# Kernel tuning notes

Hardware: AMD Instinct MI355X
Metric: run time of the kernel (lower is better)

The kernel has to match this reference:

```python
import jax, jax.numpy as jnp
import numpy as np

N_CLS = 8192
FEAT_DIM = 512
BATCH = 1024
PROTO_M = 0.95
TEMPERATURE = 0.1
BASE_TEMPERATURE = 0.1
EPS = 1e-12  # F.normalize eps


def setup_inputs() -> dict:
    key = jax.random.key(0)
    k1, k2, k3 = jax.random.split(key, 3)
    features = jax.random.normal(k1, (BATCH, FEAT_DIM), dtype=jnp.float32)
    features = features / jnp.maximum(jnp.linalg.norm(features, axis=1, keepdims=True), EPS)
    labels = jax.random.randint(k2, (BATCH,), 0, N_CLS, dtype=jnp.int64 if jax.config.jax_enable_x64 else jnp.int32)
    prototypes = jax.random.normal(k3, (N_CLS, FEAT_DIM), dtype=jnp.float32)
    prototypes = prototypes / jnp.maximum(jnp.linalg.norm(prototypes, axis=1, keepdims=True), EPS)
    return {"features": features, "labels": labels, "prototypes": prototypes}


def _l2norm_vec(v):
    # F.normalize(v, dim=0) for a 1-D vector
    return v / jnp.maximum(jnp.linalg.norm(v), EPS)


def reference(features, labels, prototypes):
    # --- sequential per-sample EMA prototype update (order matters) ---
    def step(protos, fl):
        f, l = fl
        new_p = _l2norm_vec(protos[l] * PROTO_M + f * (1.0 - PROTO_M))
        return protos.at[l].set(new_p), None

    protos, _ = jax.lax.scan(step, prototypes, (features, labels))

    # --- dispersion loss over prototype pairs ---
    logits = (protos @ protos.T) / TEMPERATURE            # [n_cls, n_cls]
    n = protos.shape[0]
    mask = 1.0 - jnp.eye(n, dtype=logits.dtype)           # off-diagonal pairs
    # log of mean exp over negatives (exactly the original, non-stabilized, form;
    # prototypes are unit-norm so |logits| <= 1/T and exp is safe)
    mean_prob_neg = jnp.log((mask * jnp.exp(logits)).sum(axis=1) / mask.sum(axis=1))
    # original drops NaN rows; with n_cls > 1 mask.sum(1) == n_cls-1 > 0 so none occur
    loss = (TEMPERATURE / BASE_TEMPERATURE) * mean_prob_neg.mean()
    return loss
```

## Files before the change

### kernel.cpp

```cpp
#include <hip/hip_runtime.h>
#include <hip/hip_fp8.h>
#include <stdint.h>

#define N_CLS 8192
#define FEAT  512
#define BATCH 1024
#define NTI   32
#define NTJ   64
#define NBLK  1056
#define NSLOT 8
#define SLOTB 24576

typedef __attribute__((ext_vector_type(4))) float f32x4;
typedef __attribute__((ext_vector_type(2))) long longx2;

__device__ inline unsigned char f2fp8(float x) {
    __hip_fp8_e4m3 q(x);
    return q.__x;
}

__global__ __launch_bounds__(256) void ema_kernel(
    const float* __restrict__ features, const int* __restrict__ labels,
    const float* __restrict__ protos,
    unsigned char* __restrict__ Phi8, float* __restrict__ rowsum) {
    const int row  = blockIdx.x * 4 + (threadIdx.x >> 6);
    const int lane = threadIdx.x & 63;
    if (lane == 0) rowsum[row] = 0.f;

    f32x4 p0 = *(const f32x4*)&protos[(size_t)row * FEAT + lane * 8];
    f32x4 p1 = *(const f32x4*)&protos[(size_t)row * FEAT + lane * 8 + 4];

    for (int c = 0; c < BATCH / 64; ++c) {
        int lab = labels[c * 64 + lane];
        unsigned long long m = __ballot(lab == row);
        while (m) {
            int b = __builtin_ctzll(m);
            m &= m - 1;
            int s = c * 64 + b;
            f32x4 f0 = *(const f32x4*)&features[(size_t)s * FEAT + lane * 8];
            f32x4 f1 = *(const f32x4*)&features[(size_t)s * FEAT + lane * 8 + 4];
            p0 = p0 * 0.95f + f0 * 0.05f;
            p1 = p1 * 0.95f + f1 * 0.05f;
            float ss = p0[0]*p0[0] + p0[1]*p0[1] + p0[2]*p0[2] + p0[3]*p0[3]
                     + p1[0]*p1[0] + p1[1]*p1[1] + p1[2]*p1[2] + p1[3]*p1[3];
            #pragma unroll
            for (int off = 32; off; off >>= 1) ss += __shfl_xor(ss, off);
            float inv = 1.0f / fmaxf(sqrtf(ss), 1e-12f);
            p0 *= inv; p1 *= inv;
        }
    }
    unsigned long long packed = 0;
    #pragma unroll
    for (int jj = 0; jj < 4; ++jj)
        packed |= (unsigned long long)f2fp8(p0[jj]) << (8 * jj);
    #pragma unroll
    for (int jj = 0; jj < 4; ++jj)
        packed |= (unsigned long long)f2fp8(p1[jj]) << (8 * (jj + 4));
    *(unsigned long long*)&Phi8[(size_t)row * FEAT + lane * 8] = packed;
}

__global__ __launch_bounds__(512, 4) void gemm_disp_kernel(
    const unsigned char* __restrict__ Phi8, float* __restrict__ rowsum) {
    __shared__ __align__(16) char smem[3 * SLOTB];

    int bid = blockIdx.x;
    int u = (bid & 7) * (NBLK / 8) + (bid >> 3);
    int i = 0;
    while (u >= NTJ - 2 * i) { u -= NTJ - 2 * i; ++i; }
    const int j = 2 * i + u;
    const bool diagovl = ((j >> 1) == i);

    const int w    = threadIdx.x >> 6;
    const int lane = threadIdx.x & 63;
    const int wr = w >> 1, wc = w & 1;
    const int h = lane >> 4;
    const int r = lane & 15;
    const int rseg = (h ^ ((r >> 1) & 3)) * 16;

    const int Ibase = i * 256, Jbase = j * 128;

    f32x4 acc[4][4];
    #pragma unroll
    for (int m = 0; m < 4; ++m)
        #pragma unroll
        for (int n = 0; n < 4; ++n) acc[m][n] = (f32x4){0.f, 0.f, 0.f, 0.f};

    const int srow = lane >> 2;
    const int sseg = (lane & 3) ^ ((lane >> 3) & 3);
    const unsigned char* gA =
        Phi8 + (size_t)(Ibase + w * 32 + srow) * FEAT + sseg * 16;
    const unsigned char* gB =
        Phi8 + (size_t)(Jbase + w * 16 + srow) * FEAT + sseg * 16;

#define STAGE(s)                                                              \
    {                                                                         \
        char* base = smem + ((s) % 3) * SLOTB;                                \
        __builtin_amdgcn_global_load_lds(                                     \
            (const __attribute__((address_space(1))) void*)(gA + (s) * 64),   \
            (__attribute__((address_space(3))) void*)(base + w * 2048),       \
            16, 0, 0);                                                        \
        __builtin_amdgcn_global_load_lds(                                     \
            (const __attribute__((address_space(1))) void*)(gA + 16 * FEAT + (s) * 64), \
            (__attribute__((address_space(3))) void*)(base + w * 2048 + 1024),\
            16, 0, 0);                                                        \
        __builtin_amdgcn_global_load_lds(                                     \
            (const __attribute__((address_space(1))) void*)(gB + (s) * 64),   \
            (__attribute__((address_space(3))) void*)(base + 16384 + w * 1024),\
            16, 0, 0);                                                        \
    }

#define MF8(ai, bi, mi, ni)                                                   \
    acc[mi][ni] = __builtin_amdgcn_mfma_f32_16x16x32_fp8_fp8(                 \
        ai[0], bi[0], acc[mi][ni], 0, 0, 0);                                  \
    acc[mi][ni] = __builtin_amdgcn_mfma_f32_16x16x32_fp8_fp8(                 \
        ai[1], bi[1], acc[mi][ni], 0, 0, 0);

#define SLOT(s, TAIL)                                                         \
    {                                                                         \
        const char* As = smem + ((s) % 3) * SLOTB;                            \
        const char* Bs = As + 16384;                                          \
        longx2 a0, a1, a2, a3, b0, b1, b2, b3;                                \
        b0 = *(const longx2*)(Bs + (wc * 64 +  0 + r) * 64 + rseg);           \
        b1 = *(const longx2*)(Bs + (wc * 64 + 16 + r) * 64 + rseg);           \
        b2 = *(const longx2*)(Bs + (wc * 64 + 32 + r) * 64 + rseg);           \
        b3 = *(const longx2*)(Bs + (wc * 64 + 48 + r) * 64 + rseg);           \
        a0 = *(const longx2*)(As + (wr * 64 +  0 + r) * 64 + rseg);           \
        a1 = *(const longx2*)(As + (wr * 64 + 16 + r) * 64 + rseg);           \
        a2 = *(const longx2*)(As + (wr * 64 + 32 + r) * 64 + rseg);           \
        a3 = *(const longx2*)(As + (wr * 64 + 48 + r) * 64 + rseg);           \
        __builtin_amdgcn_s_setprio(1);                                        \
        MF8(a0, b0, 0, 0) MF8(a1, b0, 1, 0) MF8(a2, b0, 2, 0) MF8(a3, b0, 3, 0) \
        MF8(a0, b1, 0, 1) MF8(a1, b1, 1, 1) MF8(a2, b1, 2, 1) MF8(a3, b1, 3, 1) \
        MF8(a0, b2, 0, 2) MF8(a1, b2, 1, 2) MF8(a2, b2, 2, 2) MF8(a3, b2, 3, 2) \
        MF8(a0, b3, 0, 3) MF8(a1, b3, 1, 3) MF8(a2, b3, 2, 3) MF8(a3, b3, 3, 3) \
        __builtin_amdgcn_s_setprio(0);                                        \
        TAIL                                                                  \
    }

#define TAIL_MID(s)                                                           \
    STAGE((s) + 2)                                                            \
    asm volatile("s_waitcnt vmcnt(3)" ::: "memory");                          \
    __builtin_amdgcn_s_barrier();
#define TAIL_6                                                                \
    asm volatile("s_waitcnt vmcnt(0)" ::: "memory");                          \
    __builtin_amdgcn_s_barrier();
#define TAIL_7

    STAGE(0) STAGE(1)
    asm volatile("s_waitcnt vmcnt(3)" ::: "memory");
    __builtin_amdgcn_s_barrier();

    SLOT(0, TAIL_MID(0)) SLOT(1, TAIL_MID(1)) SLOT(2, TAIL_MID(2))
    SLOT(3, TAIL_MID(3)) SLOT(4, TAIL_MID(4)) SLOT(5, TAIL_MID(5))
    SLOT(6, TAIL_6)
    SLOT(7, TAIL_7)

    #pragma unroll
    for (int m = 0; m < 4; ++m)
        #pragma unroll
        for (int n = 0; n < 4; ++n)
            #pragma unroll
            for (int q = 0; q < 4; ++q) {
                float v = __expf(acc[m][n][q] * 10.0f);
                if (diagovl &&
                    (Ibase + wr * 64 + m * 16 + h * 4 + q) ==
                    (Jbase + wc * 64 + n * 16 + r))
                    v = 0.f;
                acc[m][n][q] = v;
            }

    #pragma unroll
    for (int m = 0; m < 4; ++m) {
        float rs[4];
        #pragma unroll
        for (int q = 0; q < 4; ++q)
            rs[q] = acc[m][0][q] + acc[m][1][q] + acc[m][2][q] + acc[m][3][q];
        #pragma unroll
        for (int q = 0; q < 4; ++q)
            #pragma unroll
            for (int off = 1; off < 16; off <<= 1) rs[q] += __shfl_xor(rs[q], off);
        if (r == 0) {
            #pragma unroll
            for (int q = 0; q < 4; ++q)
                atomicAdd(&rowsum[Ibase + wr * 64 + m * 16 + h * 4 + q], rs[q]);
        }
    }

    if (!diagovl) {
        #pragma unroll
        for (int n = 0; n < 4; ++n) {
            float cs = 0.f;
            #pragma unroll
            for (int m = 0; m < 4; ++m)
                #pragma unroll
                for (int q = 0; q < 4; ++q) cs += acc[m][n][q];
            cs += __shfl_xor(cs, 16);
            cs += __shfl_xor(cs, 32);
            if (lane < 16)
                atomicAdd(&rowsum[Jbase + wc * 64 + n * 16 + r], cs);
        }
    }
}

__global__ __launch_bounds__(512) void loss_kernel(
    const float* __restrict__ rowsum, float* __restrict__ out) {
    __shared__ float red[8];
    float s = 0.f;
    for (int i = threadIdx.x; i < N_CLS; i += 512)
        s += logf(rowsum[i] * (1.0f / (float)(N_CLS - 1)));
    #pragma unroll
    for (int off = 32; off; off >>= 1) s += __shfl_xor(s, off);
    if ((threadIdx.x & 63) == 0) red[threadIdx.x >> 6] = s;
    __syncthreads();
    if (threadIdx.x == 0) {
        float tot = 0.f;
        #pragma unroll
        for (int i = 0; i < 8; ++i) tot += red[i];
        out[0] = tot * (1.0f / (float)N_CLS);
    }
}

extern "C" void kernel_launch(void* const* d_in, const int* in_sizes, int n_in,
                              void* d_out, int out_size, void* d_ws, size_t ws_size,
                              hipStream_t stream) {
    (void)in_sizes; (void)n_in; (void)out_size; (void)ws_size;
    const float* features = (const float*)d_in[0];
    const int*   labels   = (const int*)d_in[1];
    const float* protos   = (const float*)d_in[2];
    float* out = (float*)d_out;

    unsigned char* Phi8 = (unsigned char*)d_ws;
    float* rowsum = (float*)(Phi8 + (size_t)N_CLS * FEAT);

    ema_kernel<<<N_CLS / 4, 256, 0, stream>>>(features, labels, protos, Phi8, rowsum);
    gemm_disp_kernel<<<NBLK, 512, 0, stream>>>(Phi8, rowsum);
    loss_kernel<<<1, 512, 0, stream>>>(rowsum, out);
}
```

Baseline: 59.78 us.

## Split GEMM tail tiles into smaller blocks and fuse final loss reduction

The main GEMM now launches only the first 1024 tile pairs. The last 32 pairs go to a new kernel that splits each 256-row tile into four 64-row blocks, so the partial final wave is spread over more CUs. The last block of that kernel, found through an atomic done counter, computes the log-mean loss, which removes the separate loss kernel launch. The EMA loop also prefetches the next matching feature row, at the cost of more code and an atomic counter in the workspace.

New measurement: 76.20 us. +27.5%, slower.

```diff
diff --git a/kernel.cpp b/kernel.cpp
--- a/kernel.cpp
+++ b/kernel.cpp
@@ -7,9 +7,12 @@
 #define BATCH 1024
 #define NTI   32
 #define NTJ   64
-#define NBLK  1056
+#define NPAIR 1056
+#define NFULL 1024
+#define NREMP 32
 #define NSLOT 8
 #define SLOTB 24576
+#define SLOTB_R 12288
 
 typedef __attribute__((ext_vector_type(4))) float f32x4;
 typedef __attribute__((ext_vector_type(2))) long longx2;
@@ -22,10 +25,12 @@
 __global__ __launch_bounds__(256) void ema_kernel(
     const float* __restrict__ features, const int* __restrict__ labels,
     const float* __restrict__ protos,
-    unsigned char* __restrict__ Phi8, float* __restrict__ rowsum) {
+    unsigned char* __restrict__ Phi8, float* __restrict__ rowsum,
+    int* __restrict__ done) {
     const int row  = blockIdx.x * 4 + (threadIdx.x >> 6);
     const int lane = threadIdx.x & 63;
     if (lane == 0) rowsum[row] = 0.f;
+    if (blockIdx.x == 0 && threadIdx.x == 0) *done = 0;
 
     f32x4 p0 = *(const f32x4*)&protos[(size_t)row * FEAT + lane * 8];
     f32x4 p1 = *(const f32x4*)&protos[(size_t)row * FEAT + lane * 8 + 4];
@@ -33,20 +38,27 @@
     for (int c = 0; c < BATCH / 64; ++c) {
         int lab = labels[c * 64 + lane];
         unsigned long long m = __ballot(lab == row);
-        while (m) {
-            int b = __builtin_ctzll(m);
+        if (!m) continue;
+        int s = c * 64 + __builtin_ctzll(m);
+        f32x4 f0 = *(const f32x4*)&features[(size_t)s * FEAT + lane * 8];
+        f32x4 f1 = *(const f32x4*)&features[(size_t)s * FEAT + lane * 8 + 4];
+        while (true) {
             m &= m - 1;
-            int s = c * 64 + b;
-            f32x4 f0 = *(const f32x4*)&features[(size_t)s * FEAT + lane * 8];
-            f32x4 f1 = *(const f32x4*)&features[(size_t)s * FEAT + lane * 8 + 4];
-            p0 = p0 * 0.95f + f0 * 0.05f;
-            p1 = p1 * 0.95f + f1 * 0.05f;
+            f32x4 cf0 = f0, cf1 = f1;
+            if (m) {
+                int s2 = c * 64 + __builtin_ctzll(m);
+                f0 = *(const f32x4*)&features[(size_t)s2 * FEAT + lane * 8];
+                f1 = *(const f32x4*)&features[(size_t)s2 * FEAT + lane * 8 + 4];
+            }
+            p0 = p0 * 0.95f + cf0 * 0.05f;
+            p1 = p1 * 0.95f + cf1 * 0.05f;
             float ss = p0[0]*p0[0] + p0[1]*p0[1] + p0[2]*p0[2] + p0[3]*p0[3]
                      + p1[0]*p1[0] + p1[1]*p1[1] + p1[2]*p1[2] + p1[3]*p1[3];
             #pragma unroll
             for (int off = 32; off; off >>= 1) ss += __shfl_xor(ss, off);
             float inv = 1.0f / fmaxf(sqrtf(ss), 1e-12f);
             p0 *= inv; p1 *= inv;
+            if (!m) break;
         }
     }
     unsigned long long packed = 0;
@@ -64,7 +76,7 @@
     __shared__ __align__(16) char smem[3 * SLOTB];
 
     int bid = blockIdx.x;
-    int u = (bid & 7) * (NBLK / 8) + (bid >> 3);
+    int u = (bid & 7) * (NFULL / 8) + (bid >> 3);
     int i = 0;
     while (u >= NTJ - 2 * i) { u -= NTJ - 2 * i; ++i; }
     const int j = 2 * i + u;
@@ -202,21 +214,149 @@
     }
 }
 
-__global__ __launch_bounds__(512) void loss_kernel(
-    const float* __restrict__ rowsum, float* __restrict__ out) {
-    __shared__ float red[8];
-    float s = 0.f;
-    for (int i = threadIdx.x; i < N_CLS; i += 512)
-        s += logf(rowsum[i] * (1.0f / (float)(N_CLS - 1)));
-    #pragma unroll
-    for (int off = 32; off; off >>= 1) s += __shfl_xor(s, off);
-    if ((threadIdx.x & 63) == 0) red[threadIdx.x >> 6] = s;
+__global__ __launch_bounds__(256, 4) void gemm_rem_kernel(
+    const unsigned char* __restrict__ Phi8, float* __restrict__ rowsum,
+    int* __restrict__ done, float* __restrict__ out) {
+    __shared__ __align__(16) char smem[3 * SLOTB_R];
+
+    const int p  = NFULL + (blockIdx.x & 31);
+    const int qt = blockIdx.x >> 5;
+    int u = p, i = 0;
+    while (u >= NTJ - 2 * i) { u -= NTJ - 2 * i; ++i; }
+    const int j = 2 * i + u;
+    const bool diagovl = ((j >> 1) == i);
+
+    const int w    = threadIdx.x >> 6;
+    const int lane = threadIdx.x & 63;
+    const int h = lane >> 4;
+    const int r = lane & 15;
+    const int rseg = (h ^ ((r >> 1) & 3)) * 16;
+
+    const int Ibase = i * 256 + qt * 64, Jbase = j * 128;
+
+    f32x4 acc[4][2];
+    #pragma unroll
+    for (int m = 0; m < 4; ++m)
+        #pragma unroll
+        for (int n = 0; n < 2; ++n) acc[m][n] = (f32x4){0.f, 0.f, 0.f, 0.f};
+
+    const int srow = lane >> 2;
+    const int sseg = (lane & 3) ^ ((lane >> 3) & 3);
+    const unsigned char* gA =
+        Phi8 + (size_t)(Ibase + w * 16 + srow) * FEAT + sseg * 16;
+    const unsigned char* gB =
+        Phi8 + (size_t)(Jbase + w * 32 + srow) * FEAT + sseg * 16;
+
+#define STAGE_R(s)                                                            \
+    {                                                                         \
+        char* base = smem + ((s) % 3) * SLOTB_R;                              \
+        __builtin_amdgcn_global_load_lds(                                     \
+            (const __attribute__((address_space(1))) void*)(gA + (s) * 64),   \
+            (__attribute__((address_space(3))) void*)(base + w * 1024),       \
+            16, 0, 0);                                                        \
+        __builtin_amdgcn_global_load_lds(                                     \
+            (const __attribute__((address_space(1))) void*)(gB + (s) * 64),   \
+            (__attribute__((address_space(3))) void*)(base + 4096 + w * 2048),\
+            16, 0, 0);                                                        \
+        __builtin_amdgcn_global_load_lds(                                     \
+            (const __attribute__((address_space(1))) void*)(gB + 16 * FEAT + (s) * 64), \
+            (__attribute__((address_space(3))) void*)(base + 4096 + w * 2048 + 1024), \
+            16, 0, 0);                                                        \
+    }
+
+#define SLOT_R(s, TAIL)                                                       \
+    {                                                                         \
+        const char* As = smem + ((s) % 3) * SLOTB_R;                          \
+        const char* Bs = As + 4096;                                           \
+        longx2 a0, a1, a2, a3, b0, b1;                                        \
+        b0 = *(const longx2*)(Bs + (w * 32 +  0 + r) * 64 + rseg);            \
+        b1 = *(const longx2*)(Bs + (w * 32 + 16 + r) * 64 + rseg);            \
+        a0 = *(const longx2*)(As + ( 0 + r) * 64 + rseg);                     \
+        a1 = *(const longx2*)(As + (16 + r) * 64 + rseg);                     \
+        a2 = *(const longx2*)(As + (32 + r) * 64 + rseg);                     \
+        a3 = *(const longx2*)(As + (48 + r) * 64 + rseg);                     \
+        __builtin_amdgcn_s_setprio(1);                                        \
+        MF8(a0, b0, 0, 0) MF8(a1, b0, 1, 0) MF8(a2, b0, 2, 0) MF8(a3, b0, 3, 0) \
+        MF8(a0, b1, 0, 1) MF8(a1, b1, 1, 1) MF8(a2, b1, 2, 1) MF8(a3, b1, 3, 1) \
+        __builtin_amdgcn_s_setprio(0);                                        \
+        TAIL                                                                  \
+    }
+
+#define TAIL_MID_R(s)                                                         \
+    STAGE_R((s) + 2)                                                          \
+    asm volatile("s_waitcnt vmcnt(3)" ::: "memory");                          \
+    __builtin_amdgcn_s_barrier();
+
+    STAGE_R(0) STAGE_R(1)
+    asm volatile("s_waitcnt vmcnt(3)" ::: "memory");
+    __builtin_amdgcn_s_barrier();
+
+    SLOT_R(0, TAIL_MID_R(0)) SLOT_R(1, TAIL_MID_R(1)) SLOT_R(2, TAIL_MID_R(2))
+    SLOT_R(3, TAIL_MID_R(3)) SLOT_R(4, TAIL_MID_R(4)) SLOT_R(5, TAIL_MID_R(5))
+    SLOT_R(6, TAIL_6)
+    SLOT_R(7, TAIL_7)
+
+    #pragma unroll
+    for (int m = 0; m < 4; ++m)
+        #pragma unroll
+        for (int n = 0; n < 2; ++n)
+            #pragma unroll
+            for (int q = 0; q < 4; ++q) {
+                float v = __expf(acc[m][n][q] * 10.0f);
+                if ((Ibase + m * 16 + h * 4 + q) == (Jbase + w * 32 + n * 16 + r))
+                    v = 0.f;
+                acc[m][n][q] = v;
+            }
+
+    #pragma unroll
+    for (int m = 0; m < 4; ++m) {
+        float rs[4];
+        #pragma unroll
+        for (int q = 0; q < 4; ++q)
+            rs[q] = acc[m][0][q] + acc[m][1][q];
+        #pragma unroll
+        for (int q = 0; q < 4; ++q)
+            #pragma unroll
+            for (int off = 1; off < 16; off <<= 1) rs[q] += __shfl_xor(rs[q], off);
+        if (r == 0) {
+            #pragma unroll
+            for (int q = 0; q < 4; ++q)
+                atomicAdd(&rowsum[Ibase + m * 16 + h * 4 + q], rs[q]);
+        }
+    }
+
+    if (!diagovl) {
+        #pragma unroll
+        for (int n = 0; n < 2; ++n) {
+            float cs = 0.f;
+            #pragma unroll
+            for (int m = 0; m < 4; ++m)
+                #pragma unroll
+                for (int q = 0; q < 4; ++q) cs += acc[m][n][q];
+            cs += __shfl_xor(cs, 16);
+            cs += __shfl_xor(cs, 32);
+            if (lane < 16)
+                atomicAdd(&rowsum[Jbase + w * 32 + n * 16 + r], cs);
+        }
+    }
+
+    __threadfence();
+    __shared__ int islast;
+    __shared__ float red[4];
+    if (threadIdx.x == 0) islast = (atomicAdd(done, 1) == 127) ? 1 : 0;
     __syncthreads();
-    if (threadIdx.x == 0) {
-        float tot = 0.f;
-        #pragma unroll
-        for (int i = 0; i < 8; ++i) tot += red[i];
-        out[0] = tot * (1.0f / (float)N_CLS);
+    if (islast) {
+        float s = 0.f;
+        for (int idx = threadIdx.x; idx < N_CLS; idx += 256) {
+            float v = atomicAdd(&rowsum[idx], 0.0f);
+            s += logf(v * (1.0f / (float)(N_CLS - 1)));
+        }
+        #pragma unroll
+        for (int off = 32; off; off >>= 1) s += __shfl_xor(s, off);
+        if (lane == 0) red[threadIdx.x >> 6] = s;
+        __syncthreads();
+        if (threadIdx.x == 0)
+            out[0] = (red[0] + red[1] + red[2] + red[3]) * (1.0f / (float)N_CLS);
     }
 }
 
@@ -231,8 +371,10 @@
 
     unsigned char* Phi8 = (unsigned char*)d_ws;
     float* rowsum = (float*)(Phi8 + (size_t)N_CLS * FEAT);
-
-    ema_kernel<<<N_CLS / 4, 256, 0, stream>>>(features, labels, protos, Phi8, rowsum);
-    gemm_disp_kernel<<<NBLK, 512, 0, stream>>>(Phi8, rowsum);
-    loss_kernel<<<1, 512, 0, stream>>>(rowsum, out);
-}
+    int* done = (int*)(rowsum + N_CLS);
+
+    ema_kernel<<<N_CLS / 4, 256, 0, stream>>>(features, labels, protos, Phi8,
+                                              rowsum, done);
+    gemm_disp_kernel<<<NFULL, 512, 0, stream>>>(Phi8, rowsum);
+    gemm_rem_kernel<<<NREMP * 4, 256, 0, stream>>>(Phi8, rowsum, done, out);
+}
```

## Switch FP8 GEMM to 32x32x64 scaled MFMA with unit scales

Applied to the files above, without the earlier changes.

Replaces the pairs of 16x16x32 fp8 MFMAs with the MI355X 32x32x64 f8f6f4 scaled MFMA, using unit exponent scales. The LDS fragment reads, accumulator layout and the exp/mask/row-column reduction epilogue are remapped to the 32x32 output layout. The aim is fewer MFMA issues and higher matrix throughput per wave. In exchange the row reduction needs more shuffles and atomics per row, and the accumulator fragments are larger.

New measurement: 156.1 us. +161.1%, slower.

```diff
diff --git a/kernel.cpp b/kernel.cpp
--- a/kernel.cpp
+++ b/kernel.cpp
@@ -7,12 +7,15 @@
 #define BATCH 1024
 #define NTI   32
 #define NTJ   64
-#define NBLK  1056
+#define NPAIR 1056
 #define NSLOT 8
 #define SLOTB 24576
+#define UNITSC 0x7f7f7f7f
 
 typedef __attribute__((ext_vector_type(4))) float f32x4;
-typedef __attribute__((ext_vector_type(2))) long longx2;
+typedef __attribute__((ext_vector_type(16))) float f32x16;
+typedef __attribute__((ext_vector_type(4))) int i32x4;
+typedef __attribute__((ext_vector_type(8))) int i32x8;
 
 __device__ inline unsigned char f2fp8(float x) {
     __hip_fp8_e4m3 q(x);
@@ -64,7 +67,7 @@
     __shared__ __align__(16) char smem[3 * SLOTB];
 
     int bid = blockIdx.x;
-    int u = (bid & 7) * (NBLK / 8) + (bid >> 3);
+    int u = (bid & 7) * (NPAIR / 8) + (bid >> 3);
     int i = 0;
     while (u >= NTJ - 2 * i) { u -= NTJ - 2 * i; ++i; }
     const int j = 2 * i + u;
@@ -73,17 +76,18 @@
     const int w    = threadIdx.x >> 6;
     const int lane = threadIdx.x & 63;
     const int wr = w >> 1, wc = w & 1;
-    const int h = lane >> 4;
-    const int r = lane & 15;
-    const int rseg = (h ^ ((r >> 1) & 3)) * 16;
+    const int cl = lane & 31;
+    const int hf = lane >> 5;
 
     const int Ibase = i * 256, Jbase = j * 128;
 
-    f32x4 acc[4][4];
-    #pragma unroll
-    for (int m = 0; m < 4; ++m)
-        #pragma unroll
-        for (int n = 0; n < 4; ++n) acc[m][n] = (f32x4){0.f, 0.f, 0.f, 0.f};
+    f32x16 acc[2][2];
+    #pragma unroll
+    for (int m = 0; m < 2; ++m)
+        #pragma unroll
+        for (int n = 0; n < 2; ++n)
+            #pragma unroll
+            for (int t = 0; t < 16; ++t) acc[m][n][t] = 0.f;
 
     const int srow = lane >> 2;
     const int sseg = (lane & 3) ^ ((lane >> 3) & 3);
@@ -109,30 +113,33 @@
             16, 0, 0);                                                        \
     }
 
-#define MF8(ai, bi, mi, ni)                                                   \
-    acc[mi][ni] = __builtin_amdgcn_mfma_f32_16x16x32_fp8_fp8(                 \
-        ai[0], bi[0], acc[mi][ni], 0, 0, 0);                                  \
-    acc[mi][ni] = __builtin_amdgcn_mfma_f32_16x16x32_fp8_fp8(                 \
-        ai[1], bi[1], acc[mi][ni], 0, 0, 0);
+#define RDFRAG(dst, base, row)                                                \
+    {                                                                         \
+        const int swz_ = (((row) >> 1) & 3);                                  \
+        i32x4 lo_ = *(const i32x4*)((base) + (size_t)(row) * 64               \
+                                    + ((2 * hf) ^ swz_) * 16);                \
+        i32x4 hi_ = *(const i32x4*)((base) + (size_t)(row) * 64               \
+                                    + ((2 * hf + 1) ^ swz_) * 16);            \
+        _Pragma("unroll")                                                     \
+        for (int t_ = 0; t_ < 4; ++t_) { dst[t_] = lo_[t_]; dst[4 + t_] = hi_[t_]; } \
+    }
+
+#define MFS(av, bv, mi, ni)                                                   \
+    acc[mi][ni] = __builtin_amdgcn_mfma_scale_f32_32x32x64_f8f6f4(            \
+        av, bv, acc[mi][ni], 0, 0, 0, UNITSC, 0, UNITSC);
 
 #define SLOT(s, TAIL)                                                         \
     {                                                                         \
         const char* As = smem + ((s) % 3) * SLOTB;                            \
         const char* Bs = As + 16384;                                          \
-        longx2 a0, a1, a2, a3, b0, b1, b2, b3;                                \
-        b0 = *(const longx2*)(Bs + (wc * 64 +  0 + r) * 64 + rseg);           \
-        b1 = *(const longx2*)(Bs + (wc * 64 + 16 + r) * 64 + rseg);           \
-        b2 = *(const longx2*)(Bs + (wc * 64 + 32 + r) * 64 + rseg);           \
-        b3 = *(const longx2*)(Bs + (wc * 64 + 48 + r) * 64 + rseg);           \
-        a0 = *(const longx2*)(As + (wr * 64 +  0 + r) * 64 + rseg);           \
-        a1 = *(const longx2*)(As + (wr * 64 + 16 + r) * 64 + rseg);           \
-        a2 = *(const longx2*)(As + (wr * 64 + 32 + r) * 64 + rseg);           \
-        a3 = *(const longx2*)(As + (wr * 64 + 48 + r) * 64 + rseg);           \
+        i32x8 a0, a1, b0, b1;                                                 \
+        RDFRAG(b0, Bs, wc * 64 +  0 + cl)                                     \
+        RDFRAG(b1, Bs, wc * 64 + 32 + cl)                                     \
+        RDFRAG(a0, As, wr * 64 +  0 + cl)                                     \
+        RDFRAG(a1, As, wr * 64 + 32 + cl)                                     \
         __builtin_amdgcn_s_setprio(1);                                        \
-        MF8(a0, b0, 0, 0) MF8(a1, b0, 1, 0) MF8(a2, b0, 2, 0) MF8(a3, b0, 3, 0) \
-        MF8(a0, b1, 0, 1) MF8(a1, b1, 1, 1) MF8(a2, b1, 2, 1) MF8(a3, b1, 3, 1) \
-        MF8(a0, b2, 0, 2) MF8(a1, b2, 1, 2) MF8(a2, b2, 2, 2) MF8(a3, b2, 3, 2) \
-        MF8(a0, b3, 0, 3) MF8(a1, b3, 1, 3) MF8(a2, b3, 2, 3) MF8(a3, b3, 3, 3) \
+        MFS(a0, b0, 0, 0) MFS(a1, b0, 1, 0)                                   \
+        MFS(a0, b1, 0, 1) MFS(a1, b1, 1, 1)                                   \
         __builtin_amdgcn_s_setprio(0);                                        \
         TAIL                                                                  \
     }
@@ -156,48 +163,42 @@
     SLOT(7, TAIL_7)
 
     #pragma unroll
-    for (int m = 0; m < 4; ++m)
-        #pragma unroll
-        for (int n = 0; n < 4; ++n)
-            #pragma unroll
-            for (int q = 0; q < 4; ++q) {
-                float v = __expf(acc[m][n][q] * 10.0f);
-                if (diagovl &&
-                    (Ibase + wr * 64 + m * 16 + h * 4 + q) ==
-                    (Jbase + wc * 64 + n * 16 + r))
-                    v = 0.f;
-                acc[m][n][q] = v;
+    for (int m = 0; m < 2; ++m)
+        #pragma unroll
+        for (int n = 0; n < 2; ++n)
+            #pragma unroll
+            for (int t = 0; t < 16; ++t) {
+                int grow = wr * 64 + m * 32 + (t & 3) + 8 * (t >> 2) + 4 * hf;
+                int gcol = wc * 64 + n * 32 + cl;
+                float v = __expf(acc[m][n][t] * 10.0f);
+                if (diagovl && (Ibase + grow) == (Jbase + gcol)) v = 0.f;
+                acc[m][n][t] = v;
             }
 
     #pragma unroll
-    for (int m = 0; m < 4; ++m) {
-        float rs[4];
-        #pragma unroll
-        for (int q = 0; q < 4; ++q)
-            rs[q] = acc[m][0][q] + acc[m][1][q] + acc[m][2][q] + acc[m][3][q];
-        #pragma unroll
-        for (int q = 0; q < 4; ++q)
-            #pragma unroll
-            for (int off = 1; off < 16; off <<= 1) rs[q] += __shfl_xor(rs[q], off);
-        if (r == 0) {
-            #pragma unroll
-            for (int q = 0; q < 4; ++q)
-                atomicAdd(&rowsum[Ibase + wr * 64 + m * 16 + h * 4 + q], rs[q]);
+    for (int m = 0; m < 2; ++m) {
+        #pragma unroll
+        for (int t = 0; t < 16; ++t) {
+            float rs = acc[m][0][t] + acc[m][1][t];
+            #pragma unroll
+            for (int off = 1; off < 32; off <<= 1) rs += __shfl_xor(rs, off);
+            if (cl == 0)
+                atomicAdd(&rowsum[Ibase + wr * 64 + m * 32 +
+                                  (t & 3) + 8 * (t >> 2) + 4 * hf], rs);
         }
     }
 
     if (!diagovl) {
         #pragma unroll
-        for (int n = 0; n < 4; ++n) {
+        for (int n = 0; n < 2; ++n) {
             float cs = 0.f;
             #pragma unroll
-            for (int m = 0; m < 4; ++m)
+            for (int m = 0; m < 2; ++m)
                 #pragma unroll
-                for (int q = 0; q < 4; ++q) cs += acc[m][n][q];
-            cs += __shfl_xor(cs, 16);
+                for (int t = 0; t < 16; ++t) cs += acc[m][n][t];
             cs += __shfl_xor(cs, 32);
-            if (lane < 16)
-                atomicAdd(&rowsum[Jbase + wc * 64 + n * 16 + r], cs);
+            if (hf == 0)
+                atomicAdd(&rowsum[Jbase + wc * 64 + n * 32 + cl], cs);
         }
     }
 }
@@ -233,6 +234,6 @@
     float* rowsum = (float*)(Phi8 + (size_t)N_CLS * FEAT);
 
     ema_kernel<<<N_CLS / 4, 256, 0, stream>>>(features, labels, protos, Phi8, rowsum);
-    gemm_disp_kernel<<<NBLK, 512, 0, stream>>>(Phi8, rowsum);
+    gemm_disp_kernel<<<NPAIR, 512, 0, stream>>>(Phi8, rowsum);
     loss_kernel<<<1, 512, 0, stream>>>(rowsum, out);
 }
```
